# Optimization experiments

Hardware: AMD Instinct MI355X
Metric: run time of the kernel (lower is better)

## Reference

```python
import jax, jax.numpy as jnp
import numpy as np

EMBED_DIM = 64
NUM_ITEM = 1000000
BATCH = 131072
SEQ_LEN = 5
# fixed_arc = "AND,0,~1;OR,2,3;AND,5,6;OR,~7,4" parsed: (module, (pos, negated), (pos, negated))
ARC = [("AND", (0, False), (1, True)),
       ("OR",  (2, False), (3, False)),
       ("AND", (5, False), (6, False)),
       ("OR",  (7, True),  (4, False))]


def setup_inputs() -> dict:
    key = jax.random.key(0)
    ks = jax.random.split(key, 20)
    std = 0.01  # init_params: normal(0, 0.01)
    inp = {}
    inp["seq"] = jax.random.randint(ks[0], (BATCH, SEQ_LEN), 0, NUM_ITEM, dtype=jnp.int32)
    inp["pos_target"] = jax.random.randint(ks[1], (BATCH,), 0, NUM_ITEM, dtype=jnp.int32)
    inp["neg_target"] = jax.random.randint(ks[2], (BATCH,), 0, NUM_ITEM, dtype=jnp.int32)
    inp["item_embed"] = std * jax.random.normal(ks[3], (NUM_ITEM, EMBED_DIM), dtype=jnp.float32)
    t = jax.random.uniform(ks[4], (EMBED_DIM,), minval=0.0, maxval=0.1, dtype=jnp.float32)
    inp["true_vec"] = t / jnp.maximum(jnp.linalg.norm(t), 1e-12)
    inp["not_W1"] = std * jax.random.normal(ks[5], (EMBED_DIM, EMBED_DIM), dtype=jnp.float32)
    inp["not_b1"] = std * jax.random.normal(ks[6], (EMBED_DIM,), dtype=jnp.float32)
    inp["not_W2"] = std * jax.random.normal(ks[7], (EMBED_DIM, EMBED_DIM), dtype=jnp.float32)
    inp["not_b2"] = std * jax.random.normal(ks[8], (EMBED_DIM,), dtype=jnp.float32)
    inp["and_W1"] = std * jax.random.normal(ks[9], (2 * EMBED_DIM, EMBED_DIM), dtype=jnp.float32)
    inp["and_b1"] = std * jax.random.normal(ks[10], (EMBED_DIM,), dtype=jnp.float32)
    inp["and_W2"] = std * jax.random.normal(ks[11], (EMBED_DIM, EMBED_DIM), dtype=jnp.float32)
    inp["and_b2"] = std * jax.random.normal(ks[12], (EMBED_DIM,), dtype=jnp.float32)
    inp["or_W1"] = std * jax.random.normal(ks[13], (2 * EMBED_DIM, EMBED_DIM), dtype=jnp.float32)
    inp["or_b1"] = std * jax.random.normal(ks[14], (EMBED_DIM,), dtype=jnp.float32)
    inp["or_W2"] = std * jax.random.normal(ks[15], (EMBED_DIM, EMBED_DIM), dtype=jnp.float32)
    inp["or_b2"] = std * jax.random.normal(ks[16], (EMBED_DIM,), dtype=jnp.float32)
    return inp


def _mlp(x, W1, b1, W2, b2):
    # _get_ln_module(num_layers=2, dropout=0): Linear -> LeakyReLU -> Dropout(0) -> Linear
    h = jax.nn.leaky_relu(x @ W1 + b1, negative_slope=0.01)
    return h @ W2 + b2


def reference(seq, pos_target, neg_target, item_embed, true_vec,
              not_W1, not_b1, not_W2, not_b2,
              and_W1, and_b1, and_W2, and_b2,
              or_W1, or_b1, or_W2, or_b2):
    NOT = lambda x: _mlp(x, not_W1, not_b1, not_W2, not_b2)
    AND = lambda x: _mlp(x, and_W1, and_b1, and_W2, and_b2)
    OR = lambda x: _mlp(x, or_W1, or_b1, or_W2, or_b2)
    mods = {"AND": AND, "OR": OR}

    intermediates = {}

    def get_input(pos, neg):
        if pos < SEQ_LEN:
            e = item_embed[seq[:, pos]]  # [B, D] embedding gather
        else:
            e = intermediates[pos]
        return NOT(e) if neg else e

    out = None
    for layer_id, (name, (p1, n1), (p2, n2)) in enumerate(ARC):
        i1 = get_input(p1, n1)
        i2 = get_input(p2, n2)
        out = mods[name](jnp.concatenate((i1, i2), axis=-1))
        intermediates[SEQ_LEN + layer_id] = out

    enc_not = NOT(out)  # [B, D]
    pos_e = item_embed[pos_target]
    neg_e = item_embed[neg_target]
    encoded_pos = OR(jnp.concatenate((enc_not, pos_e), axis=-1))
    encoded_neg = OR(jnp.concatenate((enc_not, neg_e), axis=-1))
    encoded = jnp.concatenate((encoded_pos, encoded_neg), axis=0)  # [2B, D]

    # cosine similarity vs 'true' anchor, amplified by 10 (cos_amplify_factor)
    eps = 1e-8
    num = encoded @ true_vec
    denom = jnp.maximum(jnp.linalg.norm(encoded, axis=-1), eps) * jnp.maximum(jnp.linalg.norm(true_vec), eps)
    prediction = (num / denom) * 10.0
    return prediction
```

## Files before the change

### kernel.cpp

```cpp
#include <hip/hip_runtime.h>
#include <stdint.h>
#include <math.h>

#define BATCH 131072
#define WS_TN_OFF 65536
#define WS_B_OFF  65544

typedef __attribute__((ext_vector_type(8)))  short short8;
typedef __attribute__((ext_vector_type(16))) float float16;

union S8 { short8 s; uint32_t u[4]; };
union F8 { float f[8]; uint32_t u[8]; float4 v4[2]; };

__global__ __launch_bounds__(256)
void prep_kernel(const float* __restrict__ tvec,
                 const float* __restrict__ nW1, const float* __restrict__ nW2,
                 const float* __restrict__ aW1, const float* __restrict__ aW2,
                 const float* __restrict__ oW1, const float* __restrict__ oW2,
                 const float* __restrict__ nb1, const float* __restrict__ nb2,
                 const float* __restrict__ ab1, const float* __restrict__ ab2,
                 const float* __restrict__ ob1, const float* __restrict__ ob2,
                 char* __restrict__ ws)
{
    const int id = blockIdx.x * 256 + threadIdx.x;
    if (id == 0) {
        float s = 0.f;
        for (int j = 0; j < 64; ++j) s = fmaf(tvec[j], tvec[j], s);
        *(float*)(ws + WS_TN_OFF) = fmaxf(sqrtf(s), 1e-8f);
    }
    if (id < 32768) {
        const float* srcs[8] = { nW1, nW2, aW1, aW1 + 4096, aW2, oW1, oW1 + 4096, oW2 };
        const int u    = id >> 12;
        const int e    = id & 4095;
        const int j    = e & 7;
        const int lane = (e >> 3) & 63;
        const int f    = e >> 9;
        const int nt   = f & 1, kc = f >> 1;
        const int k    = kc * 16 + (lane >> 5) * 8 + j;
        const int n    = nt * 32 + (lane & 31);
        const uint32_t b = __float_as_uint(srcs[u][k * 64 + n]);
        const uint32_t r = b + 0x7fffu + ((b >> 16) & 1u);
        ((uint16_t*)(ws + u * 8192 + f * 1024 + lane * 16))[j] = (uint16_t)(r >> 16);
    } else if (id < 33152) {
        const int b   = id - 32768;
        const int arr = b >> 6, j = b & 63;
        const float* bp = (arr == 0) ? nb1 : (arr == 1) ? nb2 : (arr == 2) ? ab1
                        : (arr == 3) ? ab2 : (arr == 4) ? ob1 : ob2;
        ((float*)(ws + WS_B_OFF))[b] = bp[j];
    }
}

#define OPW(g,u,sH,ini,bid,ep,rd) ((g)|((u)<<3)|((sH)<<6)|((ini)<<7)|((bid)<<8)|((ep)<<11)|((rd)<<13))

__global__ __launch_bounds__(256, 3)
void logicnet_mfma(const int* __restrict__ seq, const int* __restrict__ post,
                   const int* __restrict__ negt, const float* __restrict__ E,
                   const char* __restrict__ ws, float* __restrict__ out)
{
    static const uint32_t PROG[24] = {
        OPW(3,5,0,1,4,0,0),
        OPW(4,6,0,0,0,1,0),
        OPW(0,7,0,1,5,3,0),
        OPW(2,0,0,1,0,1,0),
        OPW(0,1,0,1,1,2,0),
        OPW(0,3,0,1,2,0,0),
        OPW(1,2,0,0,0,1,0),
        OPW(0,4,0,1,3,2,0),
        OPW(0,2,0,1,2,0,0),
        OPW(0,3,1,0,0,1,0),
        OPW(0,4,0,1,3,2,0),
        OPW(0,0,0,1,0,1,0),
        OPW(0,1,0,1,1,2,0),
        OPW(0,5,0,1,4,0,0),
        OPW(5,6,0,0,0,1,0),
        OPW(0,7,0,1,5,2,0),
        OPW(0,0,0,1,0,1,0),
        OPW(0,1,0,1,1,3,0),
        OPW(0,5,1,1,4,0,0),
        OPW(6,6,0,0,0,1,0),
        OPW(0,7,0,1,5,0,1),
        OPW(0,5,1,1,4,0,0),
        OPW(7,6,0,0,0,1,0),
        OPW(0,7,0,1,5,0,2),
    };

    __shared__ uint32_t lds[4 * 3200 + 448];
    const int tid  = threadIdx.x;
    const int wid  = tid >> 6;
    const int lane = tid & 63;
    const int m    = lane & 31;
    const int h    = lane >> 5;
    const int rowbase = (blockIdx.x * 4 + wid) * 32;
    const int rr   = rowbase + m;
    uint32_t* const S0 = &lds[wid * 3200];
    uint32_t* const S1 = S0 + 2112;
    float*    const ldsb = (float*)&lds[12800];
    float*    const ltv  = (float*)&lds[13184];

    {
        const uint32_t* wsb32 = (const uint32_t*)(ws + WS_B_OFF);
        const uint32_t* tv32  = (const uint32_t*)(ws + WS_B_OFF) - 2;
        (void)tv32;
        for (int t = tid; t < 384; t += 256) lds[12800 + t] = wsb32[t];
    }
    {
        const uint32_t* tvsrc = (const uint32_t*)(ws + WS_B_OFF + 1536);
        for (int t = tid; t < 64; t += 256) lds[13184 + t] = tvsrc[t];
    }
    __syncthreads();

    const float tn = *(const float*)(ws + WS_TN_OFF);

    const int sv0 = seq[(size_t)rr * 5 + 0], sv1 = seq[(size_t)rr * 5 + 1];
    const int sv2 = seq[(size_t)rr * 5 + 2], sv3 = seq[(size_t)rr * 5 + 3];
    const int sv4 = seq[(size_t)rr * 5 + 4];
    const int ipv = post[rr], imv = negt[rr];

    float16 acc[2];

    auto gw = [&](int idx) {
        const float4* e = (const float4*)(E + (size_t)idx * 64 + h * 8);
#pragma unroll
        for (int kc = 0; kc < 4; ++kc) {
            F8 xf8;
            xf8.v4[0] = e[kc * 4];
            xf8.v4[1] = e[kc * 4 + 1];
            uint32_t pk[8];
#pragma unroll
            for (int i = 0; i < 8; ++i) {
                const uint32_t b  = xf8.u[i];
                const uint32_t hb = b & 0xffff0000u;
                const uint32_t lo = __float_as_uint(xf8.f[i] - __uint_as_float(hb));
                pk[i] = hb | (lo >> 16);
            }
            uint2* q = (uint2*)&S0[m * 66 + kc * 16 + h * 8];
            q[0] = make_uint2(pk[0], pk[1]);
            q[1] = make_uint2(pk[2], pk[3]);
            q[2] = make_uint2(pk[4], pk[5]);
            q[3] = make_uint2(pk[6], pk[7]);
        }
    };

    auto uaP = [&](int u) {
        const char* wb = ws + u * 8192 + lane * 16;
#pragma unroll
        for (int kc = 0; kc < 4; ++kc) {
            const uint2* p2 = (const uint2*)&S0[m * 66 + kc * 16 + h * 8];
            uint2 a0 = p2[0], a1 = p2[1], a2 = p2[2], a3 = p2[3];
            S8 xhi, xlo;
            xhi.u[0] = (a0.x >> 16) | (a0.y & 0xffff0000u);
            xhi.u[1] = (a1.x >> 16) | (a1.y & 0xffff0000u);
            xhi.u[2] = (a2.x >> 16) | (a2.y & 0xffff0000u);
            xhi.u[3] = (a3.x >> 16) | (a3.y & 0xffff0000u);
            xlo.u[0] = (a0.x & 0xffffu) | (a0.y << 16);
            xlo.u[1] = (a1.x & 0xffffu) | (a1.y << 16);
            xlo.u[2] = (a2.x & 0xffffu) | (a2.y << 16);
            xlo.u[3] = (a3.x & 0xffffu) | (a3.y << 16);
#pragma unroll
            for (int nt = 0; nt < 2; ++nt) {
                short8 whi = *(const short8*)(wb + (kc * 2 + nt) * 1024);
                acc[nt] = __builtin_amdgcn_mfma_f32_32x32x16_bf16(xhi.s, whi, acc[nt], 0, 0, 0);
                acc[nt] = __builtin_amdgcn_mfma_f32_32x32x16_bf16(xlo.s, whi, acc[nt], 0, 0, 0);
            }
        }
    };

    auto uaH = [&](int u) {
        const char* wb = ws + u * 8192 + lane * 16;
#pragma unroll
        for (int kc = 0; kc < 4; ++kc) {
            const uint2* p2 = (const uint2*)&S1[m * 34 + kc * 8 + h * 4];
            uint2 a0 = p2[0], a1 = p2[1];
            S8 xhi;
            xhi.u[0] = a0.x; xhi.u[1] = a0.y; xhi.u[2] = a1.x; xhi.u[3] = a1.y;
#pragma unroll
            for (int nt = 0; nt < 2; ++nt) {
                short8 whi = *(const short8*)(wb + (kc * 2 + nt) * 1024);
                acc[nt] = __builtin_amdgcn_mfma_f32_32x32x16_bf16(xhi.s, whi, acc[nt], 0, 0, 0);
            }
        }
    };

    auto epiS0 = [&](bool act) {
#pragma unroll
        for (int nt = 0; nt < 2; ++nt) {
            const int c = nt * 32 + m;
#pragma unroll
            for (int g2 = 0; g2 < 4; ++g2)
#pragma unroll
                for (int q = 0; q < 4; ++q) {
                    const int r = q + 8 * g2 + 4 * h;
                    float v = acc[nt][g2 * 4 + q];
                    if (act) v = fmaxf(v, 0.01f * v);
                    const uint32_t uu = __float_as_uint(v);
                    const uint32_t hb = uu & 0xffff0000u;
                    const uint32_t lo = __float_as_uint(v - __uint_as_float(hb));
                    S0[r * 66 + c] = hb | (lo >> 16);
                }
        }
    };

    auto epiS1 = [&]() {
        uint16_t* p = (uint16_t*)S1;
#pragma unroll
        for (int nt = 0; nt < 2; ++nt) {
            const int c = nt * 32 + m;
#pragma unroll
            for (int g2 = 0; g2 < 4; ++g2)
#pragma unroll
                for (int q = 0; q < 4; ++q) {
                    const int r = q + 8 * g2 + 4 * h;
                    const uint32_t b = __float_as_uint(acc[nt][g2 * 4 + q]);
                    const uint32_t rn = b + 0x7fffu + ((b >> 16) & 1u);
                    p[r * 68 + c] = (uint16_t)(rn >> 16);
                }
        }
    };

    auto reduce = [&](float* outp) {
#pragma unroll
        for (int nt = 0; nt < 2; ++nt) {
            const int c = nt * 32 + m;
#pragma unroll
            for (int g2 = 0; g2 < 4; ++g2)
#pragma unroll
                for (int q = 0; q < 4; ++q) {
                    const int r = q + 8 * g2 + 4 * h;
                    S0[r * 66 + c] = __float_as_uint(acc[nt][g2 * 4 + q]);
                }
        }
        float num = 0.f, ss = 0.f;
        const float* tp = ltv + h * 32;
        const uint32_t* xp = &S0[m * 66 + h * 32];
#pragma unroll
        for (int i = 0; i < 32; i += 2) {
            const float x0 = __uint_as_float(xp[i]);
            const float x1 = __uint_as_float(xp[i + 1]);
            num = fmaf(x0, tp[i], fmaf(x1, tp[i + 1], num));
            ss  = fmaf(x0, x0, fmaf(x1, x1, ss));
        }
        num += __shfl_xor(num, 32, 64);
        ss  += __shfl_xor(ss, 32, 64);
        if (h == 0) outp[m] = num / (fmaxf(sqrtf(ss), 1e-8f) * tn) * 10.0f;
    };

#pragma unroll 1
    for (int op = 0; op < 24; ++op) {
        const uint32_t cw = PROG[op];
        const int g   = cw & 7;
        const int u   = (cw >> 3) & 7;
        const int sH  = (cw >> 6) & 1;
        const int ini = (cw >> 7) & 1;
        const int bid = (cw >> 8) & 7;
        const int ep  = (cw >> 11) & 3;
        const int rd  = (cw >> 13) & 3;

        if (g) {
            int idx;
            switch (g) {
                case 1: idx = sv0; break;
                case 2: idx = sv1; break;
                case 3: idx = sv2; break;
                case 4: idx = sv3; break;
                case 5: idx = sv4; break;
                case 6: idx = ipv; break;
                default: idx = imv; break;
            }
            gw(idx);
        }
        if (ini) {
            const float b0 = ldsb[bid * 64 + m], b1 = ldsb[bid * 64 + 32 + m];
#pragma unroll
            for (int i = 0; i < 16; ++i) { acc[0][i] = b0; acc[1][i] = b1; }
        }
        if (sH) uaH(u); else uaP(u);

        if (ep == 1)      epiS0(true);
        else if (ep == 2) epiS0(false);
        else if (ep == 3) epiS1();

        if (rd == 1)      reduce(out + rowbase);
        else if (rd == 2) reduce(out + BATCH + rowbase);
    }
}

__global__ __launch_bounds__(64)
void tvec_copy(const float* __restrict__ tvec, char* __restrict__ ws) {
    const int t = threadIdx.x;
    ((float*)(ws + WS_B_OFF + 1536))[t] = tvec[t];
}

extern "C" void kernel_launch(void* const* d_in, const int* in_sizes, int n_in,
                              void* d_out, int out_size, void* d_ws, size_t ws_size,
                              hipStream_t stream) {
    const int*   seq  = (const int*)  d_in[0];
    const int*   post = (const int*)  d_in[1];
    const int*   negt = (const int*)  d_in[2];
    const float* E    = (const float*)d_in[3];
    const float* tv   = (const float*)d_in[4];
    const float* nW1  = (const float*)d_in[5];
    const float* nb1  = (const float*)d_in[6];
    const float* nW2  = (const float*)d_in[7];
    const float* nb2  = (const float*)d_in[8];
    const float* aW1  = (const float*)d_in[9];
    const float* ab1  = (const float*)d_in[10];
    const float* aW2  = (const float*)d_in[11];
    const float* ab2  = (const float*)d_in[12];
    const float* oW1  = (const float*)d_in[13];
    const float* ob1  = (const float*)d_in[14];
    const float* oW2  = (const float*)d_in[15];
    const float* ob2  = (const float*)d_in[16];
    float* out = (float*)d_out;
    char*  ws  = (char*)d_ws;

    hipLaunchKernelGGL(prep_kernel, dim3(130), dim3(256), 0, stream,
                       tv, nW1, nW2, aW1, aW2, oW1, oW2,
                       nb1, nb2, ab1, ab2, ob1, ob2, ws);
    hipLaunchKernelGGL(tvec_copy, dim3(1), dim3(64), 0, stream, tv, ws);
    hipLaunchKernelGGL(logicnet_mfma, dim3(BATCH / 128), dim3(256), 0, stream,
                       seq, post, negt, E, ws, out);
}
```

Baseline: 414.5 us.

## Keep activations in registers via swapped MFMA operands and permlane32 swaps

Swaps the MFMA operand order so the weights act as the A operand and activations as B. The accumulator layout can then be repacked into the next layer's input fragments with permlane32_swap, which removes the per-wave LDS staging buffers and the LDS round trips between layers. The tvec copy is folded into the prep kernel, dropping one launch, and the final reduction now reads accumulators directly. This raises register pressure and removes about 50KB of LDS per block, which may change occupancy under the launch bounds of 3 blocks.

```diff
diff --git a/kernel.cpp b/kernel.cpp
--- a/kernel.cpp
+++ b/kernel.cpp
@@ -8,6 +8,7 @@
 
 typedef __attribute__((ext_vector_type(8)))  short short8;
 typedef __attribute__((ext_vector_type(16))) float float16;
+typedef __attribute__((ext_vector_type(2)))  unsigned int uint2v;
 
 union S8 { short8 s; uint32_t u[4]; };
 union F8 { float f[8]; uint32_t u[8]; float4 v4[2]; };
@@ -47,10 +48,14 @@
         const float* bp = (arr == 0) ? nb1 : (arr == 1) ? nb2 : (arr == 2) ? ab1
                         : (arr == 3) ? ab2 : (arr == 4) ? ob1 : ob2;
         ((float*)(ws + WS_B_OFF))[b] = bp[j];
+    } else if (id < 33216) {
+        const int j = id - 33152;
+        ((float*)(ws + WS_B_OFF + 1536))[j] = tvec[j];
     }
 }
 
-#define OPW(g,u,sH,ini,bid,ep,rd) ((g)|((u)<<3)|((sH)<<6)|((ini)<<7)|((bid)<<8)|((ep)<<11)|((rd)<<13))
+#define OPW(g,u,sH,ini,bid,ep,rd,sl) \
+    ((g)|((u)<<3)|((sH)<<6)|((ini)<<7)|((bid)<<8)|((ep)<<11)|((rd)<<13)|((sl)<<15))
 
 __global__ __launch_bounds__(256, 3)
 void logicnet_mfma(const int* __restrict__ seq, const int* __restrict__ post,
@@ -58,33 +63,33 @@
                    const char* __restrict__ ws, float* __restrict__ out)
 {
     static const uint32_t PROG[24] = {
-        OPW(3,5,0,1,4,0,0),
-        OPW(4,6,0,0,0,1,0),
-        OPW(0,7,0,1,5,3,0),
-        OPW(2,0,0,1,0,1,0),
-        OPW(0,1,0,1,1,2,0),
-        OPW(0,3,0,1,2,0,0),
-        OPW(1,2,0,0,0,1,0),
-        OPW(0,4,0,1,3,2,0),
-        OPW(0,2,0,1,2,0,0),
-        OPW(0,3,1,0,0,1,0),
-        OPW(0,4,0,1,3,2,0),
-        OPW(0,0,0,1,0,1,0),
-        OPW(0,1,0,1,1,2,0),
-        OPW(0,5,0,1,4,0,0),
-        OPW(5,6,0,0,0,1,0),
-        OPW(0,7,0,1,5,2,0),
-        OPW(0,0,0,1,0,1,0),
-        OPW(0,1,0,1,1,3,0),
-        OPW(0,5,1,1,4,0,0),
-        OPW(6,6,0,0,0,1,0),
-        OPW(0,7,0,1,5,0,1),
-        OPW(0,5,1,1,4,0,0),
-        OPW(7,6,0,0,0,1,0),
-        OPW(0,7,0,1,5,0,2),
-    };
-
-    __shared__ uint32_t lds[4 * 3200 + 448];
+        OPW(3,5,0,1,4,0,0,0),
+        OPW(4,6,0,0,0,1,0,0),
+        OPW(0,7,0,1,5,3,0,0),
+        OPW(2,0,0,1,0,1,0,0),
+        OPW(0,1,0,1,1,2,0,0),
+        OPW(0,3,0,1,2,0,0,0),
+        OPW(1,2,0,0,0,1,0,0),
+        OPW(0,4,0,1,3,2,0,0),
+        OPW(0,2,0,1,2,0,0,0),
+        OPW(0,3,1,0,0,1,0,0),
+        OPW(0,4,0,1,3,2,0,0),
+        OPW(0,0,0,1,0,1,0,0),
+        OPW(0,1,0,1,1,2,0,0),
+        OPW(0,5,0,1,4,0,0,0),
+        OPW(5,6,0,0,0,1,0,0),
+        OPW(0,7,0,1,5,2,0,0),
+        OPW(0,0,0,1,0,1,0,0),
+        OPW(0,1,0,1,1,3,0,1),
+        OPW(0,5,1,1,4,0,0,1),
+        OPW(6,6,0,0,0,1,0,0),
+        OPW(0,7,0,1,5,0,1,0),
+        OPW(0,5,1,1,4,0,0,1),
+        OPW(7,6,0,0,0,1,0,0),
+        OPW(0,7,0,1,5,0,2,0),
+    };
+
+    __shared__ float lds[448];
     const int tid  = threadIdx.x;
     const int wid  = tid >> 6;
     const int lane = tid & 63;
@@ -92,22 +97,11 @@
     const int h    = lane >> 5;
     const int rowbase = (blockIdx.x * 4 + wid) * 32;
     const int rr   = rowbase + m;
-    uint32_t* const S0 = &lds[wid * 3200];
-    uint32_t* const S1 = S0 + 2112;
-    float*    const ldsb = (float*)&lds[12800];
-    float*    const ltv  = (float*)&lds[13184];
-
-    {
-        const uint32_t* wsb32 = (const uint32_t*)(ws + WS_B_OFF);
-        const uint32_t* tv32  = (const uint32_t*)(ws + WS_B_OFF) - 2;
-        (void)tv32;
-        for (int t = tid; t < 384; t += 256) lds[12800 + t] = wsb32[t];
-    }
-    {
-        const uint32_t* tvsrc = (const uint32_t*)(ws + WS_B_OFF + 1536);
-        for (int t = tid; t < 64; t += 256) lds[13184 + t] = tvsrc[t];
-    }
+
+    for (int t = tid; t < 448; t += 256) lds[t] = ((const float*)(ws + WS_B_OFF))[t];
     __syncthreads();
+    const float* const ldsb = lds;
+    const float* const ltv  = lds + 384;
 
     const float tn = *(const float*)(ws + WS_TN_OFF);
 
@@ -117,27 +111,24 @@
     const int ipv = post[rr], imv = negt[rr];
 
     float16 acc[2];
+    S8 xhi[4], xlo[4];
+    S8 i6f[4], encf[4];
 
     auto gw = [&](int idx) {
         const float4* e = (const float4*)(E + (size_t)idx * 64 + h * 8);
+        F8 x[4];
+#pragma unroll
+        for (int kc = 0; kc < 4; ++kc) { x[kc].v4[0] = e[kc * 4]; x[kc].v4[1] = e[kc * 4 + 1]; }
 #pragma unroll
         for (int kc = 0; kc < 4; ++kc) {
-            F8 xf8;
-            xf8.v4[0] = e[kc * 4];
-            xf8.v4[1] = e[kc * 4 + 1];
-            uint32_t pk[8];
-#pragma unroll
-            for (int i = 0; i < 8; ++i) {
-                const uint32_t b  = xf8.u[i];
-                const uint32_t hb = b & 0xffff0000u;
-                const uint32_t lo = __float_as_uint(xf8.f[i] - __uint_as_float(hb));
-                pk[i] = hb | (lo >> 16);
-            }
-            uint2* q = (uint2*)&S0[m * 66 + kc * 16 + h * 8];
-            q[0] = make_uint2(pk[0], pk[1]);
-            q[1] = make_uint2(pk[2], pk[3]);
-            q[2] = make_uint2(pk[4], pk[5]);
-            q[3] = make_uint2(pk[6], pk[7]);
+#pragma unroll
+            for (int w = 0; w < 4; ++w) {
+                const uint32_t b0 = x[kc].u[2 * w], b1 = x[kc].u[2 * w + 1];
+                xhi[kc].u[w] = __builtin_amdgcn_perm(b1, b0, 0x07060302u);
+                const float l0 = x[kc].f[2 * w]     - __uint_as_float(b0 & 0xffff0000u);
+                const float l1 = x[kc].f[2 * w + 1] - __uint_as_float(b1 & 0xffff0000u);
+                xlo[kc].u[w] = __builtin_amdgcn_perm(__float_as_uint(l1), __float_as_uint(l0), 0x07060302u);
+            }
         }
     };
 
@@ -145,100 +136,103 @@
         const char* wb = ws + u * 8192 + lane * 16;
 #pragma unroll
         for (int kc = 0; kc < 4; ++kc) {
-            const uint2* p2 = (const uint2*)&S0[m * 66 + kc * 16 + h * 8];
-            uint2 a0 = p2[0], a1 = p2[1], a2 = p2[2], a3 = p2[3];
-            S8 xhi, xlo;
-            xhi.u[0] = (a0.x >> 16) | (a0.y & 0xffff0000u);
-            xhi.u[1] = (a1.x >> 16) | (a1.y & 0xffff0000u);
-            xhi.u[2] = (a2.x >> 16) | (a2.y & 0xffff0000u);
-            xhi.u[3] = (a3.x >> 16) | (a3.y & 0xffff0000u);
-            xlo.u[0] = (a0.x & 0xffffu) | (a0.y << 16);
-            xlo.u[1] = (a1.x & 0xffffu) | (a1.y << 16);
-            xlo.u[2] = (a2.x & 0xffffu) | (a2.y << 16);
-            xlo.u[3] = (a3.x & 0xffffu) | (a3.y << 16);
-#pragma unroll
-            for (int nt = 0; nt < 2; ++nt) {
-                short8 whi = *(const short8*)(wb + (kc * 2 + nt) * 1024);
-                acc[nt] = __builtin_amdgcn_mfma_f32_32x32x16_bf16(xhi.s, whi, acc[nt], 0, 0, 0);
-                acc[nt] = __builtin_amdgcn_mfma_f32_32x32x16_bf16(xlo.s, whi, acc[nt], 0, 0, 0);
-            }
-        }
-    };
-
-    auto uaH = [&](int u) {
+            const short8 w0 = *(const short8*)(wb + (kc * 2 + 0) * 1024);
+            const short8 w1 = *(const short8*)(wb + (kc * 2 + 1) * 1024);
+            acc[0] = __builtin_amdgcn_mfma_f32_32x32x16_bf16(w0, xhi[kc].s, acc[0], 0, 0, 0);
+            acc[1] = __builtin_amdgcn_mfma_f32_32x32x16_bf16(w1, xhi[kc].s, acc[1], 0, 0, 0);
+            acc[0] = __builtin_amdgcn_mfma_f32_32x32x16_bf16(w0, xlo[kc].s, acc[0], 0, 0, 0);
+            acc[1] = __builtin_amdgcn_mfma_f32_32x32x16_bf16(w1, xlo[kc].s, acc[1], 0, 0, 0);
+        }
+    };
+
+    auto uaH = [&](int u, const S8* xf) {
         const char* wb = ws + u * 8192 + lane * 16;
 #pragma unroll
         for (int kc = 0; kc < 4; ++kc) {
-            const uint2* p2 = (const uint2*)&S1[m * 34 + kc * 8 + h * 4];
-            uint2 a0 = p2[0], a1 = p2[1];
-            S8 xhi;
-            xhi.u[0] = a0.x; xhi.u[1] = a0.y; xhi.u[2] = a1.x; xhi.u[3] = a1.y;
-#pragma unroll
-            for (int nt = 0; nt < 2; ++nt) {
-                short8 whi = *(const short8*)(wb + (kc * 2 + nt) * 1024);
-                acc[nt] = __builtin_amdgcn_mfma_f32_32x32x16_bf16(xhi.s, whi, acc[nt], 0, 0, 0);
-            }
-        }
-    };
-
-    auto epiS0 = [&](bool act) {
+            const short8 w0 = *(const short8*)(wb + (kc * 2 + 0) * 1024);
+            const short8 w1 = *(const short8*)(wb + (kc * 2 + 1) * 1024);
+            acc[0] = __builtin_amdgcn_mfma_f32_32x32x16_bf16(w0, xf[kc].s, acc[0], 0, 0, 0);
+            acc[1] = __builtin_amdgcn_mfma_f32_32x32x16_bf16(w1, xf[kc].s, acc[1], 0, 0, 0);
+        }
+    };
+
+    auto epiX = [&](bool act) {
 #pragma unroll
         for (int nt = 0; nt < 2; ++nt) {
-            const int c = nt * 32 + m;
-#pragma unroll
-            for (int g2 = 0; g2 < 4; ++g2)
-#pragma unroll
-                for (int q = 0; q < 4; ++q) {
-                    const int r = q + 8 * g2 + 4 * h;
-                    float v = acc[nt][g2 * 4 + q];
-                    if (act) v = fmaxf(v, 0.01f * v);
-                    const uint32_t uu = __float_as_uint(v);
-                    const uint32_t hb = uu & 0xffff0000u;
-                    const uint32_t lo = __float_as_uint(v - __uint_as_float(hb));
-                    S0[r * 66 + c] = hb | (lo >> 16);
-                }
-        }
-    };
-
-    auto epiS1 = [&]() {
-        uint16_t* p = (uint16_t*)S1;
+#pragma unroll
+            for (int c = 0; c < 2; ++c) {
+                uint32_t ph[2][2], pl[2][2];
+#pragma unroll
+                for (int d = 0; d < 2; ++d) {
+                    const int g2 = 2 * c + d;
+                    float v0 = acc[nt][4 * g2 + 0], v1 = acc[nt][4 * g2 + 1];
+                    float v2 = acc[nt][4 * g2 + 2], v3 = acc[nt][4 * g2 + 3];
+                    if (act) {
+                        v0 = fmaxf(v0, 0.01f * v0); v1 = fmaxf(v1, 0.01f * v1);
+                        v2 = fmaxf(v2, 0.01f * v2); v3 = fmaxf(v3, 0.01f * v3);
+                    }
+                    const uint32_t b0 = __float_as_uint(v0), b1 = __float_as_uint(v1);
+                    const uint32_t b2 = __float_as_uint(v2), b3 = __float_as_uint(v3);
+                    ph[d][0] = __builtin_amdgcn_perm(b1, b0, 0x07060302u);
+                    ph[d][1] = __builtin_amdgcn_perm(b3, b2, 0x07060302u);
+                    const float l0 = v0 - __uint_as_float(b0 & 0xffff0000u);
+                    const float l1 = v1 - __uint_as_float(b1 & 0xffff0000u);
+                    const float l2 = v2 - __uint_as_float(b2 & 0xffff0000u);
+                    const float l3 = v3 - __uint_as_float(b3 & 0xffff0000u);
+                    pl[d][0] = __builtin_amdgcn_perm(__float_as_uint(l1), __float_as_uint(l0), 0x07060302u);
+                    pl[d][1] = __builtin_amdgcn_perm(__float_as_uint(l3), __float_as_uint(l2), 0x07060302u);
+                }
+                const int kc = 2 * nt + c;
+#pragma unroll
+                for (int w = 0; w < 2; ++w) {
+                    uint2v rh = __builtin_amdgcn_permlane32_swap(ph[0][w], ph[1][w], false, false);
+                    xhi[kc].u[w]     = rh[0];
+                    xhi[kc].u[2 + w] = rh[1];
+                    uint2v rl = __builtin_amdgcn_permlane32_swap(pl[0][w], pl[1][w], false, false);
+                    xlo[kc].u[w]     = rl[0];
+                    xlo[kc].u[2 + w] = rl[1];
+                }
+            }
+        }
+    };
+
+    auto epiB = [&](S8* dst) {
 #pragma unroll
         for (int nt = 0; nt < 2; ++nt) {
-            const int c = nt * 32 + m;
-#pragma unroll
-            for (int g2 = 0; g2 < 4; ++g2)
-#pragma unroll
-                for (int q = 0; q < 4; ++q) {
-                    const int r = q + 8 * g2 + 4 * h;
-                    const uint32_t b = __float_as_uint(acc[nt][g2 * 4 + q]);
-                    const uint32_t rn = b + 0x7fffu + ((b >> 16) & 1u);
-                    p[r * 68 + c] = (uint16_t)(rn >> 16);
-                }
+#pragma unroll
+            for (int c = 0; c < 2; ++c) {
+                uint32_t pp[2][2];
+#pragma unroll
+                for (int d = 0; d < 2; ++d) {
+                    const int g2 = 2 * c + d;
+                    asm("v_cvt_pk_bf16_f32 %0, %1, %2"
+                        : "=v"(pp[d][0]) : "v"(acc[nt][4 * g2 + 0]), "v"(acc[nt][4 * g2 + 1]));
+                    asm("v_cvt_pk_bf16_f32 %0, %1, %2"
+                        : "=v"(pp[d][1]) : "v"(acc[nt][4 * g2 + 2]), "v"(acc[nt][4 * g2 + 3]));
+                }
+                const int kc = 2 * nt + c;
+#pragma unroll
+                for (int w = 0; w < 2; ++w) {
+                    uint2v r = __builtin_amdgcn_permlane32_swap(pp[0][w], pp[1][w], false, false);
+                    dst[kc].u[w]     = r[0];
+                    dst[kc].u[2 + w] = r[1];
+                }
+            }
         }
     };
 
     auto reduce = [&](float* outp) {
-#pragma unroll
-        for (int nt = 0; nt < 2; ++nt) {
-            const int c = nt * 32 + m;
-#pragma unroll
-            for (int g2 = 0; g2 < 4; ++g2)
-#pragma unroll
-                for (int q = 0; q < 4; ++q) {
-                    const int r = q + 8 * g2 + 4 * h;
-                    S0[r * 66 + c] = __float_as_uint(acc[nt][g2 * 4 + q]);
-                }
-        }
         float num = 0.f, ss = 0.f;
-        const float* tp = ltv + h * 32;
-        const uint32_t* xp = &S0[m * 66 + h * 32];
-#pragma unroll
-        for (int i = 0; i < 32; i += 2) {
-            const float x0 = __uint_as_float(xp[i]);
-            const float x1 = __uint_as_float(xp[i + 1]);
-            num = fmaf(x0, tp[i], fmaf(x1, tp[i + 1], num));
-            ss  = fmaf(x0, x0, fmaf(x1, x1, ss));
-        }
+#pragma unroll
+        for (int nt = 0; nt < 2; ++nt)
+#pragma unroll
+            for (int g2 = 0; g2 < 4; ++g2) {
+                const float4 t4 = *(const float4*)(ltv + nt * 32 + g2 * 8 + h * 4);
+                const float y0 = acc[nt][4 * g2 + 0], y1 = acc[nt][4 * g2 + 1];
+                const float y2 = acc[nt][4 * g2 + 2], y3 = acc[nt][4 * g2 + 3];
+                num = fmaf(y0, t4.x, fmaf(y1, t4.y, fmaf(y2, t4.z, fmaf(y3, t4.w, num))));
+                ss  = fmaf(y0, y0, fmaf(y1, y1, fmaf(y2, y2, fmaf(y3, y3, ss))));
+            }
         num += __shfl_xor(num, 32, 64);
         ss  += __shfl_xor(ss, 32, 64);
         if (h == 0) outp[m] = num / (fmaxf(sqrtf(ss), 1e-8f) * tn) * 10.0f;
@@ -254,6 +248,7 @@
         const int bid = (cw >> 8) & 7;
         const int ep  = (cw >> 11) & 3;
         const int rd  = (cw >> 13) & 3;
+        const int sl  = (cw >> 15) & 1;
 
         if (g) {
             int idx;
@@ -269,25 +264,25 @@
             gw(idx);
         }
         if (ini) {
-            const float b0 = ldsb[bid * 64 + m], b1 = ldsb[bid * 64 + 32 + m];
-#pragma unroll
-            for (int i = 0; i < 16; ++i) { acc[0][i] = b0; acc[1][i] = b1; }
-        }
-        if (sH) uaH(u); else uaP(u);
-
-        if (ep == 1)      epiS0(true);
-        else if (ep == 2) epiS0(false);
-        else if (ep == 3) epiS1();
+#pragma unroll
+            for (int nt = 0; nt < 2; ++nt)
+#pragma unroll
+                for (int g2 = 0; g2 < 4; ++g2) {
+                    const float4 b4 = *(const float4*)(ldsb + bid * 64 + nt * 32 + g2 * 8 + h * 4);
+                    acc[nt][4 * g2 + 0] = b4.x; acc[nt][4 * g2 + 1] = b4.y;
+                    acc[nt][4 * g2 + 2] = b4.z; acc[nt][4 * g2 + 3] = b4.w;
+                }
+        }
+        if (sH) { if (sl) uaH(u, encf); else uaH(u, i6f); }
+        else    uaP(u);
+
+        if (ep == 1)      epiX(true);
+        else if (ep == 2) epiX(false);
+        else if (ep == 3) { if (sl) epiB(encf); else epiB(i6f); }
 
         if (rd == 1)      reduce(out + rowbase);
         else if (rd == 2) reduce(out + BATCH + rowbase);
     }
-}
-
-__global__ __launch_bounds__(64)
-void tvec_copy(const float* __restrict__ tvec, char* __restrict__ ws) {
-    const int t = threadIdx.x;
-    ((float*)(ws + WS_B_OFF + 1536))[t] = tvec[t];
 }
 
 extern "C" void kernel_launch(void* const* d_in, const int* in_sizes, int n_in,
@@ -316,7 +311,6 @@
     hipLaunchKernelGGL(prep_kernel, dim3(130), dim3(256), 0, stream,
                        tv, nW1, nW2, aW1, aW2, oW1, oW2,
                        nb1, nb2, ab1, ab2, ob1, ob2, ws);
-    hipLaunchKernelGGL(tvec_copy, dim3(1), dim3(64), 0, stream, tv, ws);
     hipLaunchKernelGGL(logicnet_mfma, dim3(BATCH / 128), dim3(256), 0, stream,
                        seq, post, negt, E, ws, out);
 }
```

Result: slower. 440.8 us (+6.3%).
